# Kernel tuning notes

Measured on AMD Instinct MI355X. Metric: run time of the kernel, lower is better.

Reference implementation:

```python
import jax, jax.numpy as jnp
import numpy as np
from jax import lax

B, C, H, W = 8, 256, 64, 64
O, K, E = 256, 3, 3  # out_channels, kernel_size, num_experts

def setup_inputs() -> dict:
    key = jax.random.key(0)
    k1, k2, k3, k4, k5 = jax.random.split(key, 5)
    q = jax.random.normal(k1, (B, C, H, W), dtype=jnp.float32)
    y = jax.random.normal(k2, (B, C, H, W), dtype=jnp.float32)
    experts = jax.random.normal(k3, (E, O, 2 * C, K, K), dtype=jnp.float32)
    # torch nn.Linear(2C, E): store transposed [2C, E] for ctx @ gate_w
    bound = 1.0 / np.sqrt(2 * C)
    gate_w = jax.random.uniform(k4, (2 * C, E), minval=-bound, maxval=bound, dtype=jnp.float32)
    gate_b = jax.random.uniform(k5, (E,), minval=-bound, maxval=bound, dtype=jnp.float32)
    return {"q": q, "y": y, "experts": experts, "gate_w": gate_w, "gate_b": gate_b}

def reference(q, y, experts, gate_w, gate_b):
    # gate: softmax over experts from global-avg-pooled context of y (duplicated)
    y_ctx = jnp.mean(y, axis=(2, 3))                       # [B, C]
    context = jnp.concatenate([y_ctx, y_ctx], axis=1)       # [B, 2C]
    gates = jax.nn.softmax(context @ gate_w + gate_b, axis=1)  # [B, E]
    # per-sample fused kernel: sum_e gates[b,e] * experts[e]  -> [B, O, 2C, K, K]
    w = jnp.einsum('be,eoikl->boikl', gates, experts)
    xy = jnp.concatenate([q, q], axis=1)                     # [B, 2C, H, W]
    # batched dynamic conv via grouped conv: batch -> groups (no Python loop)
    b, c2, h, wd = xy.shape
    x1 = xy.reshape(1, b * c2, h, wd)
    w1 = w.reshape(b * O, c2, K, K)
    out = lax.conv_general_dilated(
        x1, w1, window_strides=(1, 1), padding='SAME',
        dimension_numbers=('NCHW', 'OIHW', 'NCHW'),
        feature_group_count=b)
    return out.reshape(b, O, h, wd)
```

## Files before the change

kernel.cpp:

```cpp
#include <hip/hip_runtime.h>
#include <hip/hip_bf16.h>
#include <math.h>


typedef __bf16 bf16x8 __attribute__((ext_vector_type(8)));
typedef __bf16 bf16x4 __attribute__((ext_vector_type(4)));
typedef float f32x4 __attribute__((ext_vector_type(4)));

#define AS1 __attribute__((address_space(1)))
#define AS3 __attribute__((address_space(3)))

__global__ __launch_bounds__(64) void yctx_kernel(const float* __restrict__ y,
                                                  float* __restrict__ yctx) {
  int bc = blockIdx.x;
  const float4* p = (const float4*)(y + (size_t)bc * 4096);
  int lane = threadIdx.x;
  float s = 0.f;
  for (int i = lane; i < 1024; i += 64) {
    float4 v = p[i];
    s += v.x + v.y + v.z + v.w;
  }
#pragma unroll
  for (int off = 32; off > 0; off >>= 1) s += __shfl_down(s, off, 64);
  if (lane == 0) yctx[bc] = s * (1.f / 4096.f);
}

__global__ __launch_bounds__(256) void wbuild_kernel(const float* __restrict__ experts,
                                                     const float* __restrict__ yctx,
                                                     const float* __restrict__ gw,
                                                     const float* __restrict__ gb,
                                                     __bf16* __restrict__ wf) {
  int o = blockIdx.x;
  int tid = threadIdx.x;
  __shared__ float sf[3][2304];
  __shared__ float lg[8][3];
  __shared__ float g[8][3];

  {
    int lb = tid >> 5, li = tid & 31;
    float p0 = 0.f, p1 = 0.f, p2 = 0.f;
#pragma unroll
    for (int j = 0; j < 8; j++) {
      int c = li + j * 32;
      float yv = yctx[lb * 256 + c];
      p0 += yv * (gw[c * 3 + 0] + gw[(c + 256) * 3 + 0]);
      p1 += yv * (gw[c * 3 + 1] + gw[(c + 256) * 3 + 1]);
      p2 += yv * (gw[c * 3 + 2] + gw[(c + 256) * 3 + 2]);
    }
#pragma unroll
    for (int off = 16; off > 0; off >>= 1) {
      p0 += __shfl_down(p0, off, 32);
      p1 += __shfl_down(p1, off, 32);
      p2 += __shfl_down(p2, off, 32);
    }
    if (li == 0) {
      lg[lb][0] = p0 + gb[0]; lg[lb][1] = p1 + gb[1]; lg[lb][2] = p2 + gb[2];
    }
  }

#pragma unroll
  for (int e = 0; e < 3; e++) {
    const float4* src = (const float4*)(experts + ((size_t)e * 256 + o) * 4608);
    float4* dstp = (float4*)sf[e];
    for (int i = tid; i < 576; i += 256) {
      float4 a = src[i], bq = src[i + 576];
      float4 r;
      r.x = a.x + bq.x; r.y = a.y + bq.y; r.z = a.z + bq.z; r.w = a.w + bq.w;
      dstp[i] = r;
    }
  }
  __syncthreads();
  if (tid < 8) {
    float l0 = lg[tid][0], l1 = lg[tid][1], l2 = lg[tid][2];
    float m = fmaxf(l0, fmaxf(l1, l2));
    float e0 = __expf(l0 - m), e1 = __expf(l1 - m), e2 = __expf(l2 - m);
    float inv = 1.f / (e0 + e1 + e2);
    g[tid][0] = e0 * inv; g[tid][1] = e1 * inv; g[tid][2] = e2 * inv;
  }
  __syncthreads();

  int cl = tid & 31, ch = tid >> 5;
#pragma unroll 1
  for (int b = 0; b < 8; b++) {
    float g0 = g[b][0], g1 = g[b][1], g2 = g[b][2];
#pragma unroll
    for (int tap = 0; tap < 9; tap++) {
      float v = g0 * sf[0][tid * 9 + tap] + g1 * sf[1][tid * 9 + tap] +
                g2 * sf[2][tid * 9 + tap];
      wf[((((size_t)b * 9 + tap) * 8 + ch) * 256 + o) * 32 + cl] = (__bf16)v;
    }
  }
}

__global__ __launch_bounds__(256) void qt_kernel(const float* __restrict__ q,
                                                 __bf16* __restrict__ qT) {
  int bid = blockIdx.x;
  int hp = bid % 66;
  int t2 = bid / 66;
  int ch = t2 & 7;
  int b = t2 >> 3;
  __bf16* dst = qT + (((size_t)(b * 8 + ch) * 66 + hp) * 66) * 32;
  int tid = threadIdx.x;
  float4 z4 = {0.f, 0.f, 0.f, 0.f};
  if (hp == 0 || hp == 65) {
    float4* d4 = (float4*)dst;
    for (int i = tid; i < 264; i += 256) d4[i] = z4;
    return;
  }
  __shared__ float tile2[64][33];
  int h = hp - 1;
  {
    int w = tid & 63, ci = tid >> 6;
#pragma unroll
    for (int j = 0; j < 8; j++) {
      int c = ci * 8 + j;
      tile2[w][c] = q[(((size_t)b * 256 + ch * 32 + c) * 64 + h) * 64 + w];
    }
  }
  if (tid < 4) ((float4*)dst)[tid] = z4;
  else if (tid < 8) ((float4*)(dst + 65 * 32))[tid - 4] = z4;
  __syncthreads();

  int a = tid & 7, wsl = tid >> 3;
  int cl4 = a * 4;
#pragma unroll
  for (int k = 0; k < 2; k++) {
    int w = wsl * 2 + k, wp = w + 1;
    int clp4 = (((cl4 >> 3) ^ ((wp >> 1) & 3)) << 3) | (cl4 & 7);
    float v0 = tile2[w][cl4 + 0], v1 = tile2[w][cl4 + 1];
    float v2 = tile2[w][cl4 + 2], v3 = tile2[w][cl4 + 3];
    bf16x4 r = {(__bf16)v0, (__bf16)v1, (__bf16)v2, (__bf16)v3};
    *(bf16x4*)(dst + wp * 32 + clp4) = r;
  }
}

__global__ __launch_bounds__(256) void conv_kernel(const __bf16* __restrict__ qT,
                                                   const __bf16* __restrict__ wf,
                                                   float* __restrict__ out) {
  __shared__ __align__(16) __bf16 Qlds[2][4 * 66 * 32];
  const int tid = threadIdx.x;
  const int lane = tid & 63;
  const int wv = tid >> 6;
  const int wm = wv >> 1, wn = wv & 1;
  const int l15 = lane & 15, qd = lane >> 4;

  const int bid = blockIdx.x;
  const int b = bid & 7;
  const int rem = bid >> 3;
  const int o0 = (rem >> 5) * 128;
  const int h0 = (rem & 31) * 2;

  f32x4 acc[4][4];
  {
    f32x4 z = {0.f, 0.f, 0.f, 0.f};
#pragma unroll
    for (int i = 0; i < 4; i++)
#pragma unroll
      for (int j = 0; j < 4; j++) acc[i][j] = z;
  }

  const char* qT_b = (const char*)qT + (size_t)b * 8 * 66 * 66 * 32 * 2;
  const char* abase = (const char*)wf + ((size_t)b * 9 * 8 * 256 +
                                         (size_t)(o0 + wm * 64 + l15)) * 64 +
                      (size_t)qd * 16;
  bf16x8 areg[3][4];

  {
    const char* qsrc = qT_b + ((size_t)h0) * 66 * 32 * 2;
    for (int i = tid; i < 1056; i += 256) {
      int ub = i - lane;
      __builtin_amdgcn_global_load_lds((const AS1 void*)(qsrc + ((size_t)i << 4)),
                                       (AS3 void*)((char*)Qlds[0] + ((size_t)ub << 4)),
                                       16, 0, 0);
    }
#pragma unroll
    for (int mi = 0; mi < 4; mi++) {
      areg[0][mi] = *(const bf16x8*)(abase + mi * 1024);
      areg[1][mi] = *(const bf16x8*)(abase + ((size_t)8 << 14) + mi * 1024);
    }
    __syncthreads();
  }

#pragma unroll 1
  for (int ch = 0; ch < 8; ch++) {
    const char* Qb = (const char*)Qlds[ch & 1];
    const char* qsrc_n = qT_b + ((size_t)(ch + 1) * 66 + h0) * 66 * 32 * 2;
    char* qdst_n = (char*)Qlds[(ch + 1) & 1];
#pragma unroll
    for (int tap = 0; tap < 9; tap++) {
      {
        int tapn = (tap + 2 >= 9) ? tap - 7 : tap + 2;
        int chn = (tap + 2 >= 9) ? ch + 1 : ch;
        size_t aoff = ((size_t)(tapn * 8 + chn)) << 14;
#pragma unroll
        for (int mi = 0; mi < 4; mi++)
          areg[(tap + 2) % 3][mi] = *(const bf16x8*)(abase + aoff + mi * 1024);
      }
      if (ch < 7) {
        if (tap == 0) {
          for (int i = tid; i < 512; i += 256) {
            int ub = i - lane;
            __builtin_amdgcn_global_load_lds((const AS1 void*)(qsrc_n + ((size_t)i << 4)),
                                             (AS3 void*)(qdst_n + ((size_t)ub << 4)),
                                             16, 0, 0);
          }
        } else if (tap == 1) {
          for (int i = 512 + tid; i < 1056; i += 256) {
            int ub = i - lane;
            __builtin_amdgcn_global_load_lds((const AS1 void*)(qsrc_n + ((size_t)i << 4)),
                                             (AS3 void*)(qdst_n + ((size_t)ub << 4)),
                                             16, 0, 0);
          }
        }
      }
      const int dh = tap / 3, dw = tap - dh * 3;
      const int r = wn + dh;
#pragma unroll
      for (int ni = 0; ni < 4; ni++) {
        int wp = ni * 16 + l15 + dw;
        int g = (qd ^ ((wp >> 1) & 3)) << 3;
        bf16x8 bfv = *(const bf16x8*)(Qb + ((r * 66 + wp) * 32 + g) * 2);
#pragma unroll
        for (int mi = 0; mi < 4; mi++)
          acc[mi][ni] = __builtin_amdgcn_mfma_f32_16x16x32_bf16(
              areg[tap % 3][mi], bfv, acc[mi][ni], 0, 0, 0);
      }
    }
    __syncthreads();
  }

  const int hh = h0 + wn;
#pragma unroll
  for (int mi = 0; mi < 4; mi++) {
    int o = o0 + wm * 64 + mi * 16 + qd * 4;
#pragma unroll
    for (int ni = 0; ni < 4; ni++) {
      int w = ni * 16 + l15;
#pragma unroll
      for (int rr = 0; rr < 4; rr++)
        out[(((size_t)b * 256 + (o + rr)) * 64 + hh) * 64 + w] = acc[mi][ni][rr];
    }
  }
}

extern "C" void kernel_launch(void* const* d_in, const int* in_sizes, int n_in,
                              void* d_out, int out_size, void* d_ws, size_t ws_size,
                              hipStream_t stream) {
  (void)in_sizes; (void)n_in; (void)out_size; (void)ws_size;
  const float* q = (const float*)d_in[0];
  const float* y = (const float*)d_in[1];
  const float* experts = (const float*)d_in[2];
  const float* gate_w = (const float*)d_in[3];
  const float* gate_b = (const float*)d_in[4];
  float* out = (float*)d_out;

  char* ws = (char*)d_ws;
  float* yctx = (float*)ws;
  __bf16* wf = (__bf16*)(ws + 16384);
  __bf16* qT = (__bf16*)(ws + 16384 + 9437184);

  yctx_kernel<<<2048, 64, 0, stream>>>(y, yctx);
  qt_kernel<<<8 * 8 * 66, 256, 0, stream>>>(q, qT);
  wbuild_kernel<<<256, 256, 0, stream>>>(experts, yctx, gate_w, gate_b, wf);
  conv_kernel<<<512, 256, 0, stream>>>(qT, wf, out);
}
```

Before: 178.7 us.

## Merge weight-build and q-transpose kernels; enlarge conv tile to 4 rows

Fuses the weight-build and q-transpose kernels into one launch, with a shared-memory union and blocks split by index. The conv kernel moves to 512 threads (8 waves) with each block covering 4 output rows instead of 2. Each block now stages a 6-row halo instead of 4, which cuts redundant halo loads and A-fragment reloads per output row. The grid drops to 256 blocks, which on a many-CU GPU may leave compute units idle and lower occupancy.

After: 172.2 us. 3.7% less time.

```diff
diff --git a/kernel.cpp b/kernel.cpp
--- a/kernel.cpp
+++ b/kernel.cpp
@@ -25,96 +25,107 @@
   if (lane == 0) yctx[bc] = s * (1.f / 4096.f);
 }
 
-__global__ __launch_bounds__(256) void wbuild_kernel(const float* __restrict__ experts,
-                                                     const float* __restrict__ yctx,
-                                                     const float* __restrict__ gw,
-                                                     const float* __restrict__ gb,
-                                                     __bf16* __restrict__ wf) {
-  int o = blockIdx.x;
+union PrepSmem {
+  struct {
+    float sf[3][2304];
+    float lg[8][3];
+    float g[8][3];
+  } wb;
+  float tile2[64][33];
+};
+
+__global__ __launch_bounds__(256) void prep_kernel(const float* __restrict__ q,
+                                                   const float* __restrict__ experts,
+                                                   const float* __restrict__ yctx,
+                                                   const float* __restrict__ gw,
+                                                   const float* __restrict__ gb,
+                                                   __bf16* __restrict__ qT,
+                                                   __bf16* __restrict__ wf) {
+  __shared__ PrepSmem sm;
+  int bid = blockIdx.x;
   int tid = threadIdx.x;
-  __shared__ float sf[3][2304];
-  __shared__ float lg[8][3];
-  __shared__ float g[8][3];
-
-  {
-    int lb = tid >> 5, li = tid & 31;
-    float p0 = 0.f, p1 = 0.f, p2 = 0.f;
-#pragma unroll
-    for (int j = 0; j < 8; j++) {
-      int c = li + j * 32;
-      float yv = yctx[lb * 256 + c];
-      p0 += yv * (gw[c * 3 + 0] + gw[(c + 256) * 3 + 0]);
-      p1 += yv * (gw[c * 3 + 1] + gw[(c + 256) * 3 + 1]);
-      p2 += yv * (gw[c * 3 + 2] + gw[(c + 256) * 3 + 2]);
-    }
-#pragma unroll
-    for (int off = 16; off > 0; off >>= 1) {
-      p0 += __shfl_down(p0, off, 32);
-      p1 += __shfl_down(p1, off, 32);
-      p2 += __shfl_down(p2, off, 32);
-    }
-    if (li == 0) {
-      lg[lb][0] = p0 + gb[0]; lg[lb][1] = p1 + gb[1]; lg[lb][2] = p2 + gb[2];
-    }
-  }
-
-#pragma unroll
-  for (int e = 0; e < 3; e++) {
-    const float4* src = (const float4*)(experts + ((size_t)e * 256 + o) * 4608);
-    float4* dstp = (float4*)sf[e];
-    for (int i = tid; i < 576; i += 256) {
-      float4 a = src[i], bq = src[i + 576];
-      float4 r;
-      r.x = a.x + bq.x; r.y = a.y + bq.y; r.z = a.z + bq.z; r.w = a.w + bq.w;
-      dstp[i] = r;
-    }
-  }
-  __syncthreads();
-  if (tid < 8) {
-    float l0 = lg[tid][0], l1 = lg[tid][1], l2 = lg[tid][2];
-    float m = fmaxf(l0, fmaxf(l1, l2));
-    float e0 = __expf(l0 - m), e1 = __expf(l1 - m), e2 = __expf(l2 - m);
-    float inv = 1.f / (e0 + e1 + e2);
-    g[tid][0] = e0 * inv; g[tid][1] = e1 * inv; g[tid][2] = e2 * inv;
-  }
-  __syncthreads();
-
-  int cl = tid & 31, ch = tid >> 5;
+
+  if (bid < 256) {
+    int o = bid;
+
+    {
+      int lb = tid >> 5, li = tid & 31;
+      float p0 = 0.f, p1 = 0.f, p2 = 0.f;
+#pragma unroll
+      for (int j = 0; j < 8; j++) {
+        int c = li + j * 32;
+        float yv = yctx[lb * 256 + c];
+        p0 += yv * (gw[c * 3 + 0] + gw[(c + 256) * 3 + 0]);
+        p1 += yv * (gw[c * 3 + 1] + gw[(c + 256) * 3 + 1]);
+        p2 += yv * (gw[c * 3 + 2] + gw[(c + 256) * 3 + 2]);
+      }
+#pragma unroll
+      for (int off = 16; off > 0; off >>= 1) {
+        p0 += __shfl_down(p0, off, 32);
+        p1 += __shfl_down(p1, off, 32);
+        p2 += __shfl_down(p2, off, 32);
+      }
+      if (li == 0) {
+        sm.wb.lg[lb][0] = p0 + gb[0];
+        sm.wb.lg[lb][1] = p1 + gb[1];
+        sm.wb.lg[lb][2] = p2 + gb[2];
+      }
+    }
+
+#pragma unroll
+    for (int e = 0; e < 3; e++) {
+      const float4* src = (const float4*)(experts + ((size_t)e * 256 + o) * 4608);
+      float4* dstp = (float4*)sm.wb.sf[e];
+      for (int i = tid; i < 576; i += 256) {
+        float4 a = src[i], bq = src[i + 576];
+        float4 r;
+        r.x = a.x + bq.x; r.y = a.y + bq.y; r.z = a.z + bq.z; r.w = a.w + bq.w;
+        dstp[i] = r;
+      }
+    }
+    __syncthreads();
+    if (tid < 8) {
+      float l0 = sm.wb.lg[tid][0], l1 = sm.wb.lg[tid][1], l2 = sm.wb.lg[tid][2];
+      float m = fmaxf(l0, fmaxf(l1, l2));
+      float e0 = __expf(l0 - m), e1 = __expf(l1 - m), e2 = __expf(l2 - m);
+      float inv = 1.f / (e0 + e1 + e2);
+      sm.wb.g[tid][0] = e0 * inv; sm.wb.g[tid][1] = e1 * inv; sm.wb.g[tid][2] = e2 * inv;
+    }
+    __syncthreads();
+
+    int cl = tid & 31, ch = tid >> 5;
 #pragma unroll 1
-  for (int b = 0; b < 8; b++) {
-    float g0 = g[b][0], g1 = g[b][1], g2 = g[b][2];
-#pragma unroll
-    for (int tap = 0; tap < 9; tap++) {
-      float v = g0 * sf[0][tid * 9 + tap] + g1 * sf[1][tid * 9 + tap] +
-                g2 * sf[2][tid * 9 + tap];
-      wf[((((size_t)b * 9 + tap) * 8 + ch) * 256 + o) * 32 + cl] = (__bf16)v;
-    }
-  }
-}
-
-__global__ __launch_bounds__(256) void qt_kernel(const float* __restrict__ q,
-                                                 __bf16* __restrict__ qT) {
-  int bid = blockIdx.x;
-  int hp = bid % 66;
-  int t2 = bid / 66;
+    for (int b = 0; b < 8; b++) {
+      float g0 = sm.wb.g[b][0], g1 = sm.wb.g[b][1], g2 = sm.wb.g[b][2];
+#pragma unroll
+      for (int tap = 0; tap < 9; tap++) {
+        float v = g0 * sm.wb.sf[0][tid * 9 + tap] + g1 * sm.wb.sf[1][tid * 9 + tap] +
+                  g2 * sm.wb.sf[2][tid * 9 + tap];
+        wf[((((size_t)b * 9 + tap) * 8 + ch) * 256 + o) * 32 + cl] = (__bf16)v;
+      }
+    }
+    return;
+  }
+
+  int bid2 = bid - 256;
+  int hp = bid2 % 66;
+  int t2 = bid2 / 66;
   int ch = t2 & 7;
   int b = t2 >> 3;
   __bf16* dst = qT + (((size_t)(b * 8 + ch) * 66 + hp) * 66) * 32;
-  int tid = threadIdx.x;
   float4 z4 = {0.f, 0.f, 0.f, 0.f};
   if (hp == 0 || hp == 65) {
     float4* d4 = (float4*)dst;
     for (int i = tid; i < 264; i += 256) d4[i] = z4;
     return;
   }
-  __shared__ float tile2[64][33];
   int h = hp - 1;
   {
     int w = tid & 63, ci = tid >> 6;
 #pragma unroll
     for (int j = 0; j < 8; j++) {
       int c = ci * 8 + j;
-      tile2[w][c] = q[(((size_t)b * 256 + ch * 32 + c) * 64 + h) * 64 + w];
+      sm.tile2[w][c] = q[(((size_t)b * 256 + ch * 32 + c) * 64 + h) * 64 + w];
     }
   }
   if (tid < 4) ((float4*)dst)[tid] = z4;
@@ -127,28 +138,29 @@
   for (int k = 0; k < 2; k++) {
     int w = wsl * 2 + k, wp = w + 1;
     int clp4 = (((cl4 >> 3) ^ ((wp >> 1) & 3)) << 3) | (cl4 & 7);
-    float v0 = tile2[w][cl4 + 0], v1 = tile2[w][cl4 + 1];
-    float v2 = tile2[w][cl4 + 2], v3 = tile2[w][cl4 + 3];
+    float v0 = sm.tile2[w][cl4 + 0], v1 = sm.tile2[w][cl4 + 1];
+    float v2 = sm.tile2[w][cl4 + 2], v3 = sm.tile2[w][cl4 + 3];
     bf16x4 r = {(__bf16)v0, (__bf16)v1, (__bf16)v2, (__bf16)v3};
     *(bf16x4*)(dst + wp * 32 + clp4) = r;
   }
 }
 
-__global__ __launch_bounds__(256) void conv_kernel(const __bf16* __restrict__ qT,
-                                                   const __bf16* __restrict__ wf,
-                                                   float* __restrict__ out) {
-  __shared__ __align__(16) __bf16 Qlds[2][4 * 66 * 32];
+__global__ __launch_bounds__(512, 2) void conv_kernel(const __bf16* __restrict__ qT,
+                                                      const __bf16* __restrict__ wf,
+                                                      float* __restrict__ out) {
+  __shared__ __align__(16) __bf16 Qlds[2][6 * 66 * 32];
   const int tid = threadIdx.x;
   const int lane = tid & 63;
   const int wv = tid >> 6;
-  const int wm = wv >> 1, wn = wv & 1;
+  const int wm = wv >> 2;
+  const int wn = wv & 3;
   const int l15 = lane & 15, qd = lane >> 4;
 
   const int bid = blockIdx.x;
   const int b = bid & 7;
   const int rem = bid >> 3;
-  const int o0 = (rem >> 5) * 128;
-  const int h0 = (rem & 31) * 2;
+  const int o0 = (rem >> 4) * 128;
+  const int hq = (rem & 15) * 4;
 
   f32x4 acc[4][4];
   {
@@ -166,8 +178,8 @@
   bf16x8 areg[3][4];
 
   {
-    const char* qsrc = qT_b + ((size_t)h0) * 66 * 32 * 2;
-    for (int i = tid; i < 1056; i += 256) {
+    const char* qsrc = qT_b + ((size_t)hq) * 66 * 32 * 2;
+    for (int i = tid; i < 1584; i += 512) {
       int ub = i - lane;
       __builtin_amdgcn_global_load_lds((const AS1 void*)(qsrc + ((size_t)i << 4)),
                                        (AS3 void*)((char*)Qlds[0] + ((size_t)ub << 4)),
@@ -184,7 +196,7 @@
 #pragma unroll 1
   for (int ch = 0; ch < 8; ch++) {
     const char* Qb = (const char*)Qlds[ch & 1];
-    const char* qsrc_n = qT_b + ((size_t)(ch + 1) * 66 + h0) * 66 * 32 * 2;
+    const char* qsrc_n = qT_b + ((size_t)(ch + 1) * 66 + hq) * 66 * 32 * 2;
     char* qdst_n = (char*)Qlds[(ch + 1) & 1];
 #pragma unroll
     for (int tap = 0; tap < 9; tap++) {
@@ -198,14 +210,14 @@
       }
       if (ch < 7) {
         if (tap == 0) {
-          for (int i = tid; i < 512; i += 256) {
+          for (int i = tid; i < 792; i += 512) {
             int ub = i - lane;
             __builtin_amdgcn_global_load_lds((const AS1 void*)(qsrc_n + ((size_t)i << 4)),
                                              (AS3 void*)(qdst_n + ((size_t)ub << 4)),
                                              16, 0, 0);
           }
         } else if (tap == 1) {
-          for (int i = 512 + tid; i < 1056; i += 256) {
+          for (int i = 792 + tid; i < 1584; i += 512) {
             int ub = i - lane;
             __builtin_amdgcn_global_load_lds((const AS1 void*)(qsrc_n + ((size_t)i << 4)),
                                              (AS3 void*)(qdst_n + ((size_t)ub << 4)),
@@ -229,7 +241,7 @@
     __syncthreads();
   }
 
-  const int hh = h0 + wn;
+  const int hh = hq + wn;
 #pragma unroll
   for (int mi = 0; mi < 4; mi++) {
     int o = o0 + wm * 64 + mi * 16 + qd * 4;
@@ -260,7 +272,6 @@
   __bf16* qT = (__bf16*)(ws + 16384 + 9437184);
 
   yctx_kernel<<<2048, 64, 0, stream>>>(y, yctx);
-  qt_kernel<<<8 * 8 * 66, 256, 0, stream>>>(q, qT);
-  wbuild_kernel<<<256, 256, 0, stream>>>(experts, yctx, gate_w, gate_b, wf);
-  conv_kernel<<<512, 256, 0, stream>>>(qT, wf, out);
-}
+  prep_kernel<<<256 + 4224, 256, 0, stream>>>(q, experts, yctx, gate_w, gate_b, qT, wf);
+  conv_kernel<<<256, 512, 0, stream>>>(qT, wf, out);
+}
```
